# Kernel optimization log

Hardware: AMD Instinct MI355X
Metric: run time of the kernel (lower is better)

## Reference

```python
import jax, jax.numpy as jnp
import numpy as np

# Config matching init_kwargs / input_specs
B, H, S, D = 4, 16, 4096, 64
BLK = 16          # sparsity_block
W = 32            # num_local_blocks (banded causal layout: block i attends blocks i-W+1..i)


def setup_inputs() -> dict:
    key = jax.random.key(0)
    kq, kk, kv = jax.random.split(key, 3)
    query = jax.random.normal(kq, (B, H, S, D), dtype=jnp.float16)
    k = jax.random.normal(kk, (B, H, S, D), dtype=jnp.float16)
    value = jax.random.normal(kv, (B, H, S, D), dtype=jnp.float16)
    return {"query": query, "key": k, "value": value}


def reference(query, key, value):
    b, h, s, d = query.shape
    nb = s // BLK
    scale = 1.0 / np.sqrt(d)

    qb = query.reshape(b, h, nb, BLK, d)
    kb = key.reshape(b, h, nb, BLK, d)
    vb = value.reshape(b, h, nb, BLK, d)

    # Banded causal block layout: for query block i, kv block indices i-W+1 .. i
    i = jnp.arange(nb)[:, None]                    # [nb,1]
    w = jnp.arange(W)[None, :]                     # [1,W]
    kv_idx = i - (W - 1) + w                       # [nb,W]
    valid = kv_idx >= 0
    idxc = jnp.clip(kv_idx, 0, nb - 1)

    kg = kb[:, :, idxc]                            # [B,H,nb,W,BLK,D] gathered K blocks
    vg = vb[:, :, idxc]                            # [B,H,nb,W,BLK,D]

    # SDD: block-sparse QK^T, only active blocks are computed
    scores = jnp.einsum('bhnqd,bhnwkd->bhnqwk', qb, kg).astype(jnp.float32) * scale

    # causal + validity mask on global token positions
    q_pos = (jnp.arange(nb) * BLK)[:, None, None, None] + jnp.arange(BLK)[None, :, None, None]  # [nb,BLK,1,1]
    k_pos = (kv_idx * BLK)[:, None, :, None] + jnp.arange(BLK)[None, None, None, :]             # [nb,1,W,BLK]
    mask = (k_pos <= q_pos) & valid[:, None, :, None]
    scores = jnp.where(mask, scores, -jnp.inf)

    # sparse softmax over all active key positions of each query row
    p = jax.nn.softmax(scores.reshape(b, h, nb, BLK, W * BLK), axis=-1)
    p = p.reshape(b, h, nb, BLK, W, BLK).astype(jnp.float16)

    # DSD: sparse-probabilities x dense-V
    out = jnp.einsum('bhnqwk,bhnwkd->bhnqd', p, vg)
    return out.reshape(b, h, s, d)
```

## Files before the change

### kernel.cpp

```cpp
#include <hip/hip_runtime.h>

#define SS 4096
#define DD 64
#define WW 32
#define NEG (-1e30f)
#define CSCALE 0.1803368801f

typedef _Float16 half8_t __attribute__((ext_vector_type(8)));
typedef __fp16 fp16x2_t __attribute__((ext_vector_type(2)));
typedef float float4_t __attribute__((ext_vector_type(4)));

static __device__ __forceinline__ unsigned pk(float a, float b) {
  fp16x2_t h = __builtin_amdgcn_cvt_pkrtz(a, b);
  return __builtin_bit_cast(unsigned, h);
}

static __device__ __forceinline__ half8_t cvt8s(const float* p, float c) {
  float4_t a = *(const float4_t*)p;
  float4_t b = *(const float4_t*)(p + 4);
  union { half8_t h; unsigned u[4]; } x;
  x.u[0] = pk(a[0] * c, a[1] * c);
  x.u[1] = pk(a[2] * c, a[3] * c);
  x.u[2] = pk(b[0] * c, b[1] * c);
  x.u[3] = pk(b[2] * c, b[3] * c);
  return x.h;
}

static __device__ __forceinline__ half8_t lds_frag16(const unsigned short* p) {
  union { half8_t h; uint4 u; } x;
  x.u = *(const uint4*)p;
  return x.h;
}

static __device__ __forceinline__ int ksig(int r) {
  return ((r & 3) ^ ((r >> 3) & 3)) | ((r & 2) << 1);
}

__global__ __launch_bounds__(256, 3)
void sparse_attn_kernel(const float* __restrict__ Q,
                        const float* __restrict__ K,
                        const float* __restrict__ V,
                        float* __restrict__ O) {
  extern __shared__ __align__(16) unsigned short smem[];
  unsigned short* kl = smem;
  unsigned short* vq = smem + 2 * 4096;

  const int lin = blockIdx.x;
  const int xcd = lin & 7;
  const int logical = (lin >> 3) + xcd * ((int)gridDim.x >> 3);
  const int bh = logical >> 6;
  const int i0 = (logical & 63) * 4;

  const int tid = threadIdx.x;
  const int wave = tid >> 6;
  const int lane = tid & 63;
  const int t = lane & 15;
  const int q = lane >> 4;

  const size_t base = (size_t)bh * SS * DD;
  const float* Qb = Q + base;
  const float* Kb = K + base;
  const float* Vb = V + base;

  const int i = i0 + wave;

  const float* qrow = Qb + (size_t)(i * 16 + t) * DD;
  const half8_t qf0 = cvt8s(qrow + q * 8, CSCALE);
  const half8_t qf1 = cvt8s(qrow + 32 + q * 8, CSCALE);

  const int prow0 = ((t >> 2) << 3) + (t & 3);
  int koff[2][2];
#pragma unroll
  for (int p = 0; p < 2; ++p)
#pragma unroll
    for (int ro = 0; ro < 2; ++ro) {
      const int rowb = p * 32 + prow0 + ro * 4;
      koff[p][ro] = rowb * 64 + ((q ^ ksig(rowb)) << 3);
    }
  const int voff0 = t * 64 + (((q ^ (t >> 1)) & 7) << 3);

  float4_t accO[4];
#pragma unroll
  for (int c = 0; c < 4; ++c) accO[c] = {0.f, 0.f, 0.f, 0.f};
  float l_acc = 0.0f;

  const int lo_blk = (i0 - (WW - 1)) > 0 ? (i0 - (WW - 1)) : 0;
  const int Ulo = lo_blk >> 2;
  const int Uhi = (i0 + 3) >> 2;
  const int nit = Uhi - Ulo + 1;

  const int kr_ = tid >> 2;
  const int kcg = tid & 3;
  const int kst0 = kr_ * 64 + ((((kcg * 2) ^ ksig(kr_)) & 7) << 3);
  const int kst1 = kr_ * 64 + ((((kcg * 2 + 1) ^ ksig(kr_)) & 7) << 3);

  const int vdl = tid & 31;
  const int vg8 = (tid >> 5) & 7;
  const int vst0 = (2 * vdl) * 64 + (((vg8 ^ vdl) & 7) << 3);

  const float* kg = Kb + (size_t)(Ulo * 64 + kr_) * DD + kcg * 16;
  const float* vg = Vb + (size_t)(Ulo * 64 + vg8 * 8) * DD + vdl * 2;

  float4_t kv[4];
  float2 vv[8];

  auto load_raw = [&]() {
#pragma unroll
    for (int ii = 0; ii < 4; ++ii) kv[ii] = *(const float4_t*)(kg + ii * 4);
#pragma unroll
    for (int rr = 0; rr < 8; ++rr) vv[rr] = *(const float2*)(vg + rr * DD);
    kg += 64 * DD;
    vg += 64 * DD;
  };

  auto store_stage = [&](int bf) {
    uint4 w0, w1;
    w0.x = pk(kv[0][0], kv[0][1]);
    w0.y = pk(kv[0][2], kv[0][3]);
    w0.z = pk(kv[1][0], kv[1][1]);
    w0.w = pk(kv[1][2], kv[1][3]);
    w1.x = pk(kv[2][0], kv[2][1]);
    w1.y = pk(kv[2][2], kv[2][3]);
    w1.z = pk(kv[3][0], kv[3][1]);
    w1.w = pk(kv[3][2], kv[3][3]);
    unsigned short* kd = kl + bf * 4096;
    *(uint4*)(kd + kst0) = w0;
    *(uint4*)(kd + kst1) = w1;
    uint4 wlo, whi;
    wlo.x = pk(vv[0].x, vv[1].x);
    wlo.y = pk(vv[2].x, vv[3].x);
    wlo.z = pk(vv[4].x, vv[5].x);
    wlo.w = pk(vv[6].x, vv[7].x);
    whi.x = pk(vv[0].y, vv[1].y);
    whi.y = pk(vv[2].y, vv[3].y);
    whi.z = pk(vv[4].y, vv[5].y);
    whi.w = pk(vv[6].y, vv[7].y);
    unsigned short* vd = vq + bf * 4096 + vst0;
    *(uint4*)vd = wlo;
    *(uint4*)(vd + 64) = whi;
  };

  load_raw();

  for (int it = 0; it < nit; ++it) {
    const int U = Ulo + it;
    const int bf = it & 1;
    store_stage(bf);
    __syncthreads();
    if (it + 1 < nit) load_raw();

    if (4 * U <= i && 4 * U >= i - 34) {
      const unsigned short* kd = kl + bf * 4096;
      float4_t st[4];
#pragma unroll
      for (int g = 0; g < 4; ++g) st[g] = {0.f, 0.f, 0.f, 0.f};
#pragma unroll
      for (int p = 0; p < 2; ++p)
#pragma unroll
        for (int ro = 0; ro < 2; ++ro) {
          half8_t kf0 = lds_frag16(&kd[koff[p][ro]]);
          half8_t kf1 = lds_frag16(&kd[koff[p][ro] ^ 32]);
          st[p * 2 + ro] =
              __builtin_amdgcn_mfma_f32_16x16x32_f16(kf0, qf0, st[p * 2 + ro], 0, 0, 0);
          st[p * 2 + ro] =
              __builtin_amdgcn_mfma_f32_16x16x32_f16(kf1, qf1, st[p * 2 + ro], 0, 0, 0);
        }

      float s[4][4];
      if ((4 * U < i - (WW - 1)) || (4 * U + 3 >= i)) {
#pragma unroll
        for (int p = 0; p < 2; ++p) {
          const int jj = 4 * U + 2 * p + (q >> 1);
          const bool bad = (jj < i - (WW - 1)) || (jj > i);
          const bool dg = (jj == i);
          const int kr = (q & 1) << 3;
#pragma unroll
          for (int ro = 0; ro < 2; ++ro)
#pragma unroll
            for (int r = 0; r < 4; ++r) {
              float v = st[p * 2 + ro][r];
              if (bad || (dg && (kr + ro * 4 + r > t))) v = NEG;
              s[p * 2 + ro][r] = v;
            }
        }
      } else {
#pragma unroll
        for (int g = 0; g < 4; ++g)
#pragma unroll
          for (int r = 0; r < 4; ++r) s[g][r] = st[g][r];
      }

#pragma unroll
      for (int g = 0; g < 4; ++g)
#pragma unroll
        for (int r = 0; r < 4; ++r) {
          s[g][r] = __builtin_exp2f(s[g][r]);
          l_acc += s[g][r];
        }

      union { half8_t h; unsigned u[4]; } pb0, pb1;
      pb0.u[0] = pk(s[0][0], s[0][1]);
      pb0.u[1] = pk(s[0][2], s[0][3]);
      pb0.u[2] = pk(s[1][0], s[1][1]);
      pb0.u[3] = pk(s[1][2], s[1][3]);
      pb1.u[0] = pk(s[2][0], s[2][1]);
      pb1.u[1] = pk(s[2][2], s[2][3]);
      pb1.u[2] = pk(s[3][0], s[3][1]);
      pb1.u[3] = pk(s[3][2], s[3][3]);

      const unsigned short* vd = vq + bf * 4096;
#pragma unroll
      for (int c = 0; c < 4; ++c) {
        const int vo = c * 1024 + voff0;
        half8_t va0 = lds_frag16(&vd[vo]);
        half8_t va1 = lds_frag16(&vd[vo ^ 32]);
        accO[c] = __builtin_amdgcn_mfma_f32_16x16x32_f16(va0, pb0.h, accO[c], 0, 0, 0);
        accO[c] = __builtin_amdgcn_mfma_f32_16x16x32_f16(va1, pb1.h, accO[c], 0, 0, 0);
      }
    }
  }

  float l_run = l_acc;
  l_run += __shfl_xor(l_run, 16);
  l_run += __shfl_xor(l_run, 32);
  const float inv_l = 1.0f / l_run;
  float* orow = O + base + (size_t)(i * 16 + t) * DD;
#pragma unroll
  for (int c = 0; c < 4; ++c) {
    float4_t ov;
#pragma unroll
    for (int r = 0; r < 4; ++r) ov[r] = accO[c][r] * inv_l;
    *(float4_t*)(orow + c * 16 + q * 4) = ov;
  }
}

extern "C" void kernel_launch(void* const* d_in, const int* in_sizes, int n_in,
                              void* d_out, int out_size, void* d_ws, size_t ws_size,
                              hipStream_t stream) {
  const float* Q = (const float*)d_in[0];
  const float* K = (const float*)d_in[1];
  const float* V = (const float*)d_in[2];
  float* O = (float*)d_out;
  sparse_attn_kernel<<<dim3(4096), dim3(256), 49152, stream>>>(Q, K, V, O);
}
```

Baseline: 254.4 us.

## Split kv iterations across two wave groups per block with LDS reduction

Doubles the block to 512 threads, where two groups of four waves process alternating kv tiles for the same query blocks. Each thread's staging load shrinks accordingly. The partial output accumulators and row sums are then combined through shared memory before the final normalize and store. The aim is more waves in flight to hide global-load and MFMA latency. The cost is an extra barrier, a shared-memory reduction, and half the waves idling during the epilogue.

```diff
diff --git a/kernel.cpp b/kernel.cpp
--- a/kernel.cpp
+++ b/kernel.cpp
@@ -36,7 +36,7 @@
   return ((r & 3) ^ ((r >> 3) & 3)) | ((r & 2) << 1);
 }
 
-__global__ __launch_bounds__(256, 3)
+__global__ __launch_bounds__(512, 6)
 void sparse_attn_kernel(const float* __restrict__ Q,
                         const float* __restrict__ K,
                         const float* __restrict__ V,
@@ -53,6 +53,8 @@
 
   const int tid = threadIdx.x;
   const int wave = tid >> 6;
+  const int wq = wave & 3;
+  const int h = wave >> 2;
   const int lane = tid & 63;
   const int t = lane & 15;
   const int q = lane >> 4;
@@ -62,7 +64,7 @@
   const float* Kb = K + base;
   const float* Vb = V + base;
 
-  const int i = i0 + wave;
+  const int i = i0 + wq;
 
   const float* qrow = Qb + (size_t)(i * 16 + t) * DD;
   const half8_t qf0 = cvt8s(qrow + q * 8, CSCALE);
@@ -89,55 +91,45 @@
   const int Uhi = (i0 + 3) >> 2;
   const int nit = Uhi - Ulo + 1;
 
-  const int kr_ = tid >> 2;
-  const int kcg = tid & 3;
-  const int kst0 = kr_ * 64 + ((((kcg * 2) ^ ksig(kr_)) & 7) << 3);
-  const int kst1 = kr_ * 64 + ((((kcg * 2 + 1) ^ ksig(kr_)) & 7) << 3);
+  const int kr_ = tid >> 3;
+  const int kc8 = tid & 7;
+  const int kst0 = kr_ * 64 + ((kc8 ^ ksig(kr_)) << 3);
 
   const int vdl = tid & 31;
-  const int vg8 = (tid >> 5) & 7;
-  const int vst0 = (2 * vdl) * 64 + (((vg8 ^ vdl) & 7) << 3);
-
-  const float* kg = Kb + (size_t)(Ulo * 64 + kr_) * DD + kcg * 16;
-  const float* vg = Vb + (size_t)(Ulo * 64 + vg8 * 8) * DD + vdl * 2;
-
-  float4_t kv[4];
-  float2 vv[8];
+  const int vng = tid >> 5;
+  const int vst0 =
+      (2 * vdl) * 64 + ((((vng >> 1) ^ vdl) & 7) << 3) + (vng & 1) * 4;
+
+  const float* kg = Kb + (size_t)(Ulo * 64 + kr_) * DD + kc8 * 8;
+  const float* vg = Vb + (size_t)(Ulo * 64 + vng * 4) * DD + vdl * 2;
+
+  float4_t kv[2];
+  float2 vv[4];
 
   auto load_raw = [&]() {
-#pragma unroll
-    for (int ii = 0; ii < 4; ++ii) kv[ii] = *(const float4_t*)(kg + ii * 4);
-#pragma unroll
-    for (int rr = 0; rr < 8; ++rr) vv[rr] = *(const float2*)(vg + rr * DD);
+    kv[0] = *(const float4_t*)kg;
+    kv[1] = *(const float4_t*)(kg + 4);
+#pragma unroll
+    for (int rr = 0; rr < 4; ++rr) vv[rr] = *(const float2*)(vg + rr * DD);
     kg += 64 * DD;
     vg += 64 * DD;
   };
 
   auto store_stage = [&](int bf) {
-    uint4 w0, w1;
-    w0.x = pk(kv[0][0], kv[0][1]);
-    w0.y = pk(kv[0][2], kv[0][3]);
-    w0.z = pk(kv[1][0], kv[1][1]);
-    w0.w = pk(kv[1][2], kv[1][3]);
-    w1.x = pk(kv[2][0], kv[2][1]);
-    w1.y = pk(kv[2][2], kv[2][3]);
-    w1.z = pk(kv[3][0], kv[3][1]);
-    w1.w = pk(kv[3][2], kv[3][3]);
-    unsigned short* kd = kl + bf * 4096;
-    *(uint4*)(kd + kst0) = w0;
-    *(uint4*)(kd + kst1) = w1;
-    uint4 wlo, whi;
+    uint4 w;
+    w.x = pk(kv[0][0], kv[0][1]);
+    w.y = pk(kv[0][2], kv[0][3]);
+    w.z = pk(kv[1][0], kv[1][1]);
+    w.w = pk(kv[1][2], kv[1][3]);
+    *(uint4*)(kl + bf * 4096 + kst0) = w;
+    uint2 wlo, whi;
     wlo.x = pk(vv[0].x, vv[1].x);
     wlo.y = pk(vv[2].x, vv[3].x);
-    wlo.z = pk(vv[4].x, vv[5].x);
-    wlo.w = pk(vv[6].x, vv[7].x);
     whi.x = pk(vv[0].y, vv[1].y);
     whi.y = pk(vv[2].y, vv[3].y);
-    whi.z = pk(vv[4].y, vv[5].y);
-    whi.w = pk(vv[6].y, vv[7].y);
     unsigned short* vd = vq + bf * 4096 + vst0;
-    *(uint4*)vd = wlo;
-    *(uint4*)(vd + 64) = whi;
+    *(uint2*)vd = wlo;
+    *(uint2*)(vd + 64) = whi;
   };
 
   load_raw();
@@ -149,7 +141,7 @@
     __syncthreads();
     if (it + 1 < nit) load_raw();
 
-    if (4 * U <= i && 4 * U >= i - 34) {
+    if (4 * U <= i && 4 * U >= i - 34 && (it & 1) == h) {
       const unsigned short* kd = kl + bf * 4096;
       float4_t st[4];
 #pragma unroll
@@ -220,17 +212,34 @@
     }
   }
 
-  float l_run = l_acc;
-  l_run += __shfl_xor(l_run, 16);
-  l_run += __shfl_xor(l_run, 32);
-  const float inv_l = 1.0f / l_run;
-  float* orow = O + base + (size_t)(i * 16 + t) * DD;
-#pragma unroll
-  for (int c = 0; c < 4; ++c) {
-    float4_t ov;
-#pragma unroll
-    for (int r = 0; r < 4; ++r) ov[r] = accO[c][r] * inv_l;
-    *(float4_t*)(orow + c * 16 + q * 4) = ov;
+  __syncthreads();
+  float* red = (float*)smem;
+  const int ridx = (wq * 64 + lane) * 17;
+  if (h == 1) {
+#pragma unroll
+    for (int c = 0; c < 4; ++c)
+#pragma unroll
+      for (int r = 0; r < 4; ++r) red[ridx + c * 4 + r] = accO[c][r];
+    red[ridx + 16] = l_acc;
+  }
+  __syncthreads();
+  if (h == 0) {
+#pragma unroll
+    for (int c = 0; c < 4; ++c)
+#pragma unroll
+      for (int r = 0; r < 4; ++r) accO[c][r] += red[ridx + c * 4 + r];
+    float l_run = l_acc + red[ridx + 16];
+    l_run += __shfl_xor(l_run, 16);
+    l_run += __shfl_xor(l_run, 32);
+    const float inv_l = 1.0f / l_run;
+    float* orow = O + base + (size_t)(i * 16 + t) * DD;
+#pragma unroll
+    for (int c = 0; c < 4; ++c) {
+      float4_t ov;
+#pragma unroll
+      for (int r = 0; r < 4; ++r) ov[r] = accO[c][r] * inv_l;
+      *(float4_t*)(orow + c * 16 + q * 4) = ov;
+    }
   }
 }
 
@@ -241,5 +250,5 @@
   const float* K = (const float*)d_in[1];
   const float* V = (const float*)d_in[2];
   float* O = (float*)d_out;
-  sparse_attn_kernel<<<dim3(4096), dim3(256), 49152, stream>>>(Q, K, V, O);
-}
+  sparse_attn_kernel<<<dim3(4096), dim3(512), 49152, stream>>>(Q, K, V, O);
+}
```

New measurement: 303.8 us. +19.4%, slower.

## Process two query blocks per wave to reuse staged K/V tiles

Applied to the files above, without the earlier changes.

Each wave now computes two adjacent query blocks, so a workgroup covers eight query blocks and the grid is halved. Every K/V tile loaded, converted and staged in shared memory is reused by twice as many query blocks, cutting global traffic and fp32-to-fp16 conversion per output. In exchange it doubles accumulator and score registers, lowers the occupancy target to two blocks per CU, and raises dynamic shared memory allocation.

```diff
diff --git a/kernel.cpp b/kernel.cpp
--- a/kernel.cpp
+++ b/kernel.cpp
@@ -36,7 +36,7 @@
   return ((r & 3) ^ ((r >> 3) & 3)) | ((r & 2) << 1);
 }
 
-__global__ __launch_bounds__(256, 3)
+__global__ __launch_bounds__(256, 2)
 void sparse_attn_kernel(const float* __restrict__ Q,
                         const float* __restrict__ K,
                         const float* __restrict__ V,
@@ -48,8 +48,8 @@
   const int lin = blockIdx.x;
   const int xcd = lin & 7;
   const int logical = (lin >> 3) + xcd * ((int)gridDim.x >> 3);
-  const int bh = logical >> 6;
-  const int i0 = (logical & 63) * 4;
+  const int bh = logical >> 5;
+  const int i0 = (logical & 31) * 8;
 
   const int tid = threadIdx.x;
   const int wave = tid >> 6;
@@ -62,11 +62,15 @@
   const float* Kb = K + base;
   const float* Vb = V + base;
 
-  const int i = i0 + wave;
-
-  const float* qrow = Qb + (size_t)(i * 16 + t) * DD;
-  const half8_t qf0 = cvt8s(qrow + q * 8, CSCALE);
-  const half8_t qf1 = cvt8s(qrow + 32 + q * 8, CSCALE);
+  const int iA = i0 + 2 * wave;
+  const int iB = iA + 1;
+
+  const float* qrowA = Qb + (size_t)(iA * 16 + t) * DD;
+  const half8_t qfA0 = cvt8s(qrowA + q * 8, CSCALE);
+  const half8_t qfA1 = cvt8s(qrowA + 32 + q * 8, CSCALE);
+  const float* qrowB = Qb + (size_t)(iB * 16 + t) * DD;
+  const half8_t qfB0 = cvt8s(qrowB + q * 8, CSCALE);
+  const half8_t qfB1 = cvt8s(qrowB + 32 + q * 8, CSCALE);
 
   const int prow0 = ((t >> 2) << 3) + (t & 3);
   int koff[2][2];
@@ -79,14 +83,17 @@
     }
   const int voff0 = t * 64 + (((q ^ (t >> 1)) & 7) << 3);
 
-  float4_t accO[4];
-#pragma unroll
-  for (int c = 0; c < 4; ++c) accO[c] = {0.f, 0.f, 0.f, 0.f};
-  float l_acc = 0.0f;
+  float4_t accA[4], accB[4];
+#pragma unroll
+  for (int c = 0; c < 4; ++c) {
+    accA[c] = {0.f, 0.f, 0.f, 0.f};
+    accB[c] = {0.f, 0.f, 0.f, 0.f};
+  }
+  float lA = 0.0f, lB = 0.0f;
 
   const int lo_blk = (i0 - (WW - 1)) > 0 ? (i0 - (WW - 1)) : 0;
   const int Ulo = lo_blk >> 2;
-  const int Uhi = (i0 + 3) >> 2;
+  const int Uhi = (i0 + 7) >> 2;
   const int nit = Uhi - Ulo + 1;
 
   const int kr_ = tid >> 2;
@@ -149,64 +156,84 @@
     __syncthreads();
     if (it + 1 < nit) load_raw();
 
-    if (4 * U <= i && 4 * U >= i - 34) {
+    const int U4 = 4 * U;
+    if (U4 <= iB && U4 >= iA - 34) {
       const unsigned short* kd = kl + bf * 4096;
-      float4_t st[4];
-#pragma unroll
-      for (int g = 0; g < 4; ++g) st[g] = {0.f, 0.f, 0.f, 0.f};
+      float4_t stA[4], stB[4];
+#pragma unroll
+      for (int g = 0; g < 4; ++g) {
+        stA[g] = {0.f, 0.f, 0.f, 0.f};
+        stB[g] = {0.f, 0.f, 0.f, 0.f};
+      }
 #pragma unroll
       for (int p = 0; p < 2; ++p)
 #pragma unroll
         for (int ro = 0; ro < 2; ++ro) {
           half8_t kf0 = lds_frag16(&kd[koff[p][ro]]);
           half8_t kf1 = lds_frag16(&kd[koff[p][ro] ^ 32]);
-          st[p * 2 + ro] =
-              __builtin_amdgcn_mfma_f32_16x16x32_f16(kf0, qf0, st[p * 2 + ro], 0, 0, 0);
-          st[p * 2 + ro] =
-              __builtin_amdgcn_mfma_f32_16x16x32_f16(kf1, qf1, st[p * 2 + ro], 0, 0, 0);
+          const int g = p * 2 + ro;
+          stA[g] = __builtin_amdgcn_mfma_f32_16x16x32_f16(kf0, qfA0, stA[g], 0, 0, 0);
+          stA[g] = __builtin_amdgcn_mfma_f32_16x16x32_f16(kf1, qfA1, stA[g], 0, 0, 0);
+          stB[g] = __builtin_amdgcn_mfma_f32_16x16x32_f16(kf0, qfB0, stB[g], 0, 0, 0);
+          stB[g] = __builtin_amdgcn_mfma_f32_16x16x32_f16(kf1, qfB1, stB[g], 0, 0, 0);
         }
 
-      float s[4][4];
-      if ((4 * U < i - (WW - 1)) || (4 * U + 3 >= i)) {
+      float sA[4][4], sB[4][4];
+      if (U4 >= iA - 30 && U4 + 3 < iA) {
+#pragma unroll
+        for (int g = 0; g < 4; ++g)
+#pragma unroll
+          for (int r = 0; r < 4; ++r) {
+            sA[g][r] = stA[g][r];
+            sB[g][r] = stB[g][r];
+          }
+      } else {
 #pragma unroll
         for (int p = 0; p < 2; ++p) {
-          const int jj = 4 * U + 2 * p + (q >> 1);
-          const bool bad = (jj < i - (WW - 1)) || (jj > i);
-          const bool dg = (jj == i);
+          const int jj = U4 + 2 * p + (q >> 1);
           const int kr = (q & 1) << 3;
 #pragma unroll
           for (int ro = 0; ro < 2; ++ro)
 #pragma unroll
             for (int r = 0; r < 4; ++r) {
-              float v = st[p * 2 + ro][r];
-              if (bad || (dg && (kr + ro * 4 + r > t))) v = NEG;
-              s[p * 2 + ro][r] = v;
+              const int g = p * 2 + ro;
+              float vA = stA[g][r], vB = stB[g][r];
+              const bool dgm = (kr + ro * 4 + r > t);
+              if ((jj < iA - (WW - 1)) || (jj > iA) || (jj == iA && dgm)) vA = NEG;
+              if ((jj < iB - (WW - 1)) || (jj > iB) || (jj == iB && dgm)) vB = NEG;
+              sA[g][r] = vA;
+              sB[g][r] = vB;
             }
         }
-      } else {
-#pragma unroll
-        for (int g = 0; g < 4; ++g)
-#pragma unroll
-          for (int r = 0; r < 4; ++r) s[g][r] = st[g][r];
       }
 
 #pragma unroll
       for (int g = 0; g < 4; ++g)
 #pragma unroll
         for (int r = 0; r < 4; ++r) {
-          s[g][r] = __builtin_exp2f(s[g][r]);
-          l_acc += s[g][r];
+          sA[g][r] = __builtin_exp2f(sA[g][r]);
+          lA += sA[g][r];
+          sB[g][r] = __builtin_exp2f(sB[g][r]);
+          lB += sB[g][r];
         }
 
-      union { half8_t h; unsigned u[4]; } pb0, pb1;
-      pb0.u[0] = pk(s[0][0], s[0][1]);
-      pb0.u[1] = pk(s[0][2], s[0][3]);
-      pb0.u[2] = pk(s[1][0], s[1][1]);
-      pb0.u[3] = pk(s[1][2], s[1][3]);
-      pb1.u[0] = pk(s[2][0], s[2][1]);
-      pb1.u[1] = pk(s[2][2], s[2][3]);
-      pb1.u[2] = pk(s[3][0], s[3][1]);
-      pb1.u[3] = pk(s[3][2], s[3][3]);
+      union { half8_t h; unsigned u[4]; } pA0, pA1, pB0, pB1;
+      pA0.u[0] = pk(sA[0][0], sA[0][1]);
+      pA0.u[1] = pk(sA[0][2], sA[0][3]);
+      pA0.u[2] = pk(sA[1][0], sA[1][1]);
+      pA0.u[3] = pk(sA[1][2], sA[1][3]);
+      pA1.u[0] = pk(sA[2][0], sA[2][1]);
+      pA1.u[1] = pk(sA[2][2], sA[2][3]);
+      pA1.u[2] = pk(sA[3][0], sA[3][1]);
+      pA1.u[3] = pk(sA[3][2], sA[3][3]);
+      pB0.u[0] = pk(sB[0][0], sB[0][1]);
+      pB0.u[1] = pk(sB[0][2], sB[0][3]);
+      pB0.u[2] = pk(sB[1][0], sB[1][1]);
+      pB0.u[3] = pk(sB[1][2], sB[1][3]);
+      pB1.u[0] = pk(sB[2][0], sB[2][1]);
+      pB1.u[1] = pk(sB[2][2], sB[2][3]);
+      pB1.u[2] = pk(sB[3][0], sB[3][1]);
+      pB1.u[3] = pk(sB[3][2], sB[3][3]);
 
       const unsigned short* vd = vq + bf * 4096;
 #pragma unroll
@@ -214,23 +241,37 @@
         const int vo = c * 1024 + voff0;
         half8_t va0 = lds_frag16(&vd[vo]);
         half8_t va1 = lds_frag16(&vd[vo ^ 32]);
-        accO[c] = __builtin_amdgcn_mfma_f32_16x16x32_f16(va0, pb0.h, accO[c], 0, 0, 0);
-        accO[c] = __builtin_amdgcn_mfma_f32_16x16x32_f16(va1, pb1.h, accO[c], 0, 0, 0);
+        accA[c] = __builtin_amdgcn_mfma_f32_16x16x32_f16(va0, pA0.h, accA[c], 0, 0, 0);
+        accA[c] = __builtin_amdgcn_mfma_f32_16x16x32_f16(va1, pA1.h, accA[c], 0, 0, 0);
+        accB[c] = __builtin_amdgcn_mfma_f32_16x16x32_f16(va0, pB0.h, accB[c], 0, 0, 0);
+        accB[c] = __builtin_amdgcn_mfma_f32_16x16x32_f16(va1, pB1.h, accB[c], 0, 0, 0);
       }
     }
   }
 
-  float l_run = l_acc;
-  l_run += __shfl_xor(l_run, 16);
-  l_run += __shfl_xor(l_run, 32);
-  const float inv_l = 1.0f / l_run;
-  float* orow = O + base + (size_t)(i * 16 + t) * DD;
+  float lAr = lA;
+  lAr += __shfl_xor(lAr, 16);
+  lAr += __shfl_xor(lAr, 32);
+  const float invA = 1.0f / lAr;
+  float* orowA = O + base + (size_t)(iA * 16 + t) * DD;
 #pragma unroll
   for (int c = 0; c < 4; ++c) {
     float4_t ov;
 #pragma unroll
-    for (int r = 0; r < 4; ++r) ov[r] = accO[c][r] * inv_l;
-    *(float4_t*)(orow + c * 16 + q * 4) = ov;
+    for (int r = 0; r < 4; ++r) ov[r] = accA[c][r] * invA;
+    *(float4_t*)(orowA + c * 16 + q * 4) = ov;
+  }
+  float lBr = lB;
+  lBr += __shfl_xor(lBr, 16);
+  lBr += __shfl_xor(lBr, 32);
+  const float invB = 1.0f / lBr;
+  float* orowB = O + base + (size_t)(iB * 16 + t) * DD;
+#pragma unroll
+  for (int c = 0; c < 4; ++c) {
+    float4_t ov;
+#pragma unroll
+    for (int r = 0; r < 4; ++r) ov[r] = accB[c][r] * invB;
+    *(float4_t*)(orowB + c * 16 + q * 4) = ov;
   }
 }
 
@@ -241,5 +282,5 @@
   const float* K = (const float*)d_in[1];
   const float* V = (const float*)d_in[2];
   float* O = (float*)d_out;
-  sparse_attn_kernel<<<dim3(4096), dim3(256), 49152, stream>>>(Q, K, V, O);
-}
+  sparse_attn_kernel<<<dim3(2048), dim3(256), 65536, stream>>>(Q, K, V, O);
+}
```

After: 252.4 us. Within noise of the previous version (-0.8%).
